# Kernel tuning notes

Hardware: AMD Instinct MI355X
Metric: run time of the kernel (lower is better)

## Reference

```python
import jax, jax.numpy as jnp
import numpy as np

SIZE = 1024        # number of neurons
INPUT = 1024       # input_size (previous layer width)
CTX = 512          # context_size
CMS = 4            # context_map_size -> 2**4 = 16 weight rows per neuron
BATCH = 256
LR = 0.01
PCLIP = 0.01       # pred_clipping
WCLIP = 5.0        # weight_clipping


def _logit(x):
    return jnp.log(x) - jnp.log1p(-x)


def setup_inputs() -> dict:
    key = jax.random.key(0)
    k1, k2, k3, k4, k5, k6 = jax.random.split(key, 6)
    logits = jax.random.normal(k1, (INPUT, BATCH), jnp.float32)
    context_inputs = jax.random.normal(k2, (CTX, BATCH), jnp.float32)
    targets = jax.random.uniform(k3, (BATCH,), jnp.float32)
    context_maps = jax.random.normal(k4, (SIZE, CMS, CTX), jnp.float32)
    context_maps = context_maps / jnp.linalg.norm(context_maps, axis=2, keepdims=True)
    context_bias = jax.random.normal(k5, (SIZE, CMS, 1), jnp.float32)
    lo = _logit(jnp.float32(PCLIP))
    hi = _logit(jnp.float32(1.0 - PCLIP))
    bias = jax.random.uniform(k6, (1,), jnp.float32, lo, hi)
    weights = jnp.full((SIZE, 2 ** CMS, INPUT), 1.0 / INPUT, jnp.float32)
    return dict(logits=logits, context_inputs=context_inputs, targets=targets,
                weights=weights, context_maps=context_maps,
                context_bias=context_bias, bias=bias)


def reference(logits, context_inputs, targets, weights, context_maps, context_bias, bias):
    # --- context hashing: which of the 2^CMS weight rows each (neuron, sample) uses ---
    # distances: (size, cms, batch)
    distances = jnp.einsum('smc,cb->smb', context_maps, context_inputs)
    bits = (distances > context_bias).astype(jnp.int32)
    conv = (2 ** jnp.arange(CMS, dtype=jnp.int32))[None, :, None]
    idx = jnp.sum(bits * conv, axis=1)                 # (size, batch) in [0, 2^CMS)

    rows = jnp.arange(SIZE)[:, None]                   # (size, 1)
    sel = weights[rows, idx]                           # gathered weights (size, batch, input)

    lo = _logit(jnp.float32(PCLIP))
    hi = _logit(jnp.float32(1.0 - PCLIP))
    # torch does matmul(sel, logits).diagonal(dim1=1,dim2=2); the diagonal is exactly
    # the per-sample dot product, computed here directly without the (size,b,b) waste.
    out = jnp.clip(jnp.einsum('sbi,ib->sb', sel, logits), lo, hi)
    out = out.at[0].set(bias[0])                       # bias overrides neuron 0

    # --- online weight update (targets provided) ---
    sig = jax.nn.sigmoid(out)                          # (size, batch)
    upd = LR * (sig - targets[None, :])[:, :, None] * logits.T[None, :, :]  # (size,b,input)
    new_weights = weights.at[rows, idx].set(jnp.clip(sel - upd, -WCLIP, WCLIP))

    return jnp.squeeze(out), new_weights
```

## Files before the change

kernel.cpp:

```cpp
#include <hip/hip_runtime.h>

#define LRC   0.01f
#define WCLIP 5.0f
#define LO   (-4.5951198501345898f)
#define HI   ( 4.5951198501345898f)

__device__ __forceinline__ unsigned short f2bf(float f) {
    unsigned int u = __float_as_uint(f);
    u += 0x7fffu + ((u >> 16) & 1u);
    return (unsigned short)(u >> 16);
}
__device__ __forceinline__ float bflo(unsigned int p) { return __uint_as_float(p << 16); }
__device__ __forceinline__ float bfhi(unsigned int p) { return __uint_as_float(p & 0xffff0000u); }

__global__ __launch_bounds__(256) void k1_idx_lt(
    const float* __restrict__ cmap,
    const float* __restrict__ ctx,
    const float* __restrict__ cbias,
    const float* __restrict__ logits,
    int*   __restrict__ idxb,
    float* __restrict__ lT)
{
    __shared__ __align__(16) float As[64 * 68];
    __shared__ __align__(16) float Bs[64 * 68];
    const int t   = threadIdx.x;
    const int blk = blockIdx.x;

    if (blk < 256) {
        const int gm = blk >> 2, gn = blk & 3;
        const int m0 = gm << 6, n0 = gn << 6;
        const int tm = t >> 4, tn = t & 15;

        const int rs = t >> 4;
        const int cs = (t & 15) << 2;

        float acc[4][4];
        #pragma unroll
        for (int i = 0; i < 4; i++)
            #pragma unroll
            for (int j = 0; j < 4; j++) acc[i][j] = 0.f;

        float4 va[4], vb[4];
        #pragma unroll
        for (int rep = 0; rep < 4; rep++) {
            va[rep] = *(const float4*)(cmap + (m0 + (rep << 4) + rs) * 512 + cs);
            vb[rep] = *(const float4*)(ctx + (((rep << 4) + rs)) * 256 + n0 + cs);
        }

        for (int k0 = 0; k0 < 512; k0 += 64) {
            __syncthreads();
            #pragma unroll
            for (int rep = 0; rep < 4; rep++) {
                const int r = (rep << 4) + rs;
                As[(cs + 0) * 68 + r] = va[rep].x;
                As[(cs + 1) * 68 + r] = va[rep].y;
                As[(cs + 2) * 68 + r] = va[rep].z;
                As[(cs + 3) * 68 + r] = va[rep].w;
                *(float4*)(Bs + r * 68 + cs) = vb[rep];
            }
            if (k0 + 64 < 512) {
                #pragma unroll
                for (int rep = 0; rep < 4; rep++) {
                    va[rep] = *(const float4*)(cmap + (m0 + (rep << 4) + rs) * 512 + k0 + 64 + cs);
                    vb[rep] = *(const float4*)(ctx + (k0 + 64 + (rep << 4) + rs) * 256 + n0 + cs);
                }
            }
            __syncthreads();

            const float* ap = As + (tm << 2);
            const float* bp = Bs + (tn << 2);
            #pragma unroll 8
            for (int k = 0; k < 64; ++k) {
                float4 a4 = *(const float4*)(ap + k * 68);
                float4 b4 = *(const float4*)(bp + k * 68);
                acc[0][0] = fmaf(a4.x, b4.x, acc[0][0]);
                acc[0][1] = fmaf(a4.x, b4.y, acc[0][1]);
                acc[0][2] = fmaf(a4.x, b4.z, acc[0][2]);
                acc[0][3] = fmaf(a4.x, b4.w, acc[0][3]);
                acc[1][0] = fmaf(a4.y, b4.x, acc[1][0]);
                acc[1][1] = fmaf(a4.y, b4.y, acc[1][1]);
                acc[1][2] = fmaf(a4.y, b4.z, acc[1][2]);
                acc[1][3] = fmaf(a4.y, b4.w, acc[1][3]);
                acc[2][0] = fmaf(a4.z, b4.x, acc[2][0]);
                acc[2][1] = fmaf(a4.z, b4.y, acc[2][1]);
                acc[2][2] = fmaf(a4.z, b4.z, acc[2][2]);
                acc[2][3] = fmaf(a4.z, b4.w, acc[2][3]);
                acc[3][0] = fmaf(a4.w, b4.x, acc[3][0]);
                acc[3][1] = fmaf(a4.w, b4.y, acc[3][1]);
                acc[3][2] = fmaf(a4.w, b4.z, acc[3][2]);
                acc[3][3] = fmaf(a4.w, b4.w, acc[3][3]);
            }
        }
        const int s = (gm << 4) + tm;
        int4 iv;
        int* ivp = &iv.x;
        float cb[4];
        #pragma unroll
        for (int i = 0; i < 4; i++) cb[i] = cbias[(s << 2) + i];
        #pragma unroll
        for (int j = 0; j < 4; j++) {
            int v = 0;
            #pragma unroll
            for (int i = 0; i < 4; i++)
                v |= (acc[i][j] > cb[i]) ? (1 << i) : 0;
            ivp[j] = v;
        }
        *(int4*)(idxb + s * 256 + n0 + (tn << 2)) = iv;
    } else {
        float* T = As;
        const int bi = blk - 256;
        const int i0 = (bi >> 2) << 6;
        const int b0 = (bi & 3) << 6;
        #pragma unroll
        for (int rep = 0; rep < 4; rep++) {
            int flat4 = rep * 256 + t;
            int r = flat4 >> 4;
            int c = (flat4 & 15) << 2;
            float4 v = *(const float4*)(logits + (i0 + r) * 256 + b0 + c);
            T[(c + 0) * 68 + r] = v.x;
            T[(c + 1) * 68 + r] = v.y;
            T[(c + 2) * 68 + r] = v.z;
            T[(c + 3) * 68 + r] = v.w;
        }
        __syncthreads();
        #pragma unroll
        for (int rep = 0; rep < 4; rep++) {
            int flat4 = rep * 256 + t;
            int r = flat4 >> 4;
            int c = (flat4 & 15) << 2;
            *(float4*)(lT + (b0 + r) * 1024 + i0 + c) =
                *(const float4*)(T + r * 68 + c);
        }
    }
}

#define WSTRIDE 514

__global__ __launch_bounds__(1024, 8) void k2_fwd_upd(
    const float* __restrict__ logits,
    const float* __restrict__ targets,
    const float* __restrict__ weights,
    const float* __restrict__ bias,
    const int*   __restrict__ idxb,
    const float* __restrict__ lT,
    float* __restrict__ outp,
    float* __restrict__ outw)
{
    __shared__ __align__(16) unsigned int wlds[32 * WSTRIDE];
    __shared__ float red[3 * 2 * 256];
    __shared__ float sig_lds[2 * 256];
    __shared__ int   lastb[32];
    __shared__ float cf_lds[32];

    const int t  = threadIdx.x;
    const int b  = t & 255;
    const int q  = t >> 8;
    const int s0 = blockIdx.x << 1;

    if (t < 32) lastb[t] = -1;

    int jg[2], rowoff[2];
    #pragma unroll
    for (int g = 0; g < 2; g++) {
        jg[g] = idxb[(s0 + g) * 256 + b];
        rowoff[g] = ((g << 4) + jg[g]) * WSTRIDE;
    }

    #pragma unroll
    for (int seg = 0; seg < 8; ++seg) {
        const int flat4 = (seg << 10) + t;
        const int r  = flat4 >> 8;
        const int c4 = (flat4 & 255) << 2;
        float4 v = *(const float4*)(weights +
                      ((size_t)(s0 + (r >> 4)) << 14) + ((r & 15) << 10) + c4);
        unsigned int p0 = (unsigned int)f2bf(v.x) | ((unsigned int)f2bf(v.y) << 16);
        unsigned int p1 = (unsigned int)f2bf(v.z) | ((unsigned int)f2bf(v.w) << 16);
        *(uint2*)(wlds + r * WSTRIDE + (c4 >> 1)) = make_uint2(p0, p1);
    }
    __syncthreads();

    float acc[2] = {0.f, 0.f};
    const int qq = q << 4;
    for (int c0 = 0; c0 < 16; ++c0) {
        const int ibase = (c0 << 6) + qq;
        #pragma unroll
        for (int ii = 0; ii < 16; ii += 4) {
            const int i = ibase + ii;
            float l0 = logits[(i + 0) * 256 + b];
            float l1 = logits[(i + 1) * 256 + b];
            float l2 = logits[(i + 2) * 256 + b];
            float l3 = logits[(i + 3) * 256 + b];
            #pragma unroll
            for (int g = 0; g < 2; g++) {
                uint2 wp = *(const uint2*)(wlds + rowoff[g] + (i >> 1));
                acc[g] = fmaf(bflo(wp.x), l0, acc[g]);
                acc[g] = fmaf(bfhi(wp.x), l1, acc[g]);
                acc[g] = fmaf(bflo(wp.y), l2, acc[g]);
                acc[g] = fmaf(bfhi(wp.y), l3, acc[g]);
            }
        }
    }

    if (q > 0) {
        #pragma unroll
        for (int g = 0; g < 2; g++) red[((q - 1) * 2 + g) * 256 + b] = acc[g];
    }
    __syncthreads();
    if (q == 0) {
        #pragma unroll
        for (int g = 0; g < 2; g++) {
            float tot = acc[g] + red[(0 * 2 + g) * 256 + b]
                               + red[(1 * 2 + g) * 256 + b]
                               + red[(2 * 2 + g) * 256 + b];
            float outv = fminf(fmaxf(tot, LO), HI);
            if (s0 + g == 0) outv = bias[0];
            outp[(s0 + g) * 256 + b] = outv;
            sig_lds[(g << 8) + b] = 1.f / (1.f + __expf(-outv));
            atomicMax(&lastb[(g << 4) + jg[g]], b);
        }
    }
    __syncthreads();
    if (t < 32) {
        int g  = t >> 4;
        int bb = lastb[t];
        float cfv = 0.f;
        if (bb >= 0) cfv = LRC * (sig_lds[(g << 8) + bb] - targets[bb]);
        cf_lds[t] = cfv;
    }
    __syncthreads();

    const int er = t >> 5;
    const int ec = (t & 31) << 2;
    const size_t rowbase = ((size_t)(s0 + (er >> 4)) << 14) + ((size_t)(er & 15) << 10);
    const int   col = lastb[er];
    const float cf  = cf_lds[er];
    const float* lrow = lT + ((size_t)(col < 0 ? 0 : col) << 10);
    const unsigned int* wrow = wlds + er * WSTRIDE;
    #pragma unroll 4
    for (int seg = 0; seg < 8; ++seg) {
        const int c2 = ec + (seg << 7);
        uint2 wp = *(const uint2*)(wrow + (c2 >> 1));
        float4 res = make_float4(bflo(wp.x), bfhi(wp.x), bflo(wp.y), bfhi(wp.y));
        if (col >= 0) {
            float4 lv = *(const float4*)(lrow + c2);
            res.x = fminf(fmaxf(res.x - cf * lv.x, -WCLIP), WCLIP);
            res.y = fminf(fmaxf(res.y - cf * lv.y, -WCLIP), WCLIP);
            res.z = fminf(fmaxf(res.z - cf * lv.z, -WCLIP), WCLIP);
            res.w = fminf(fmaxf(res.w - cf * lv.w, -WCLIP), WCLIP);
        }
        *(float4*)(outw + rowbase + c2) = res;
    }
}

extern "C" void kernel_launch(void* const* d_in, const int* in_sizes, int n_in,
                              void* d_out, int out_size, void* d_ws, size_t ws_size,
                              hipStream_t stream) {
    const float* logits  = (const float*)d_in[0];
    const float* ctx     = (const float*)d_in[1];
    const float* targets = (const float*)d_in[2];
    const float* weights = (const float*)d_in[3];
    const float* cmap    = (const float*)d_in[4];
    const float* cbias   = (const float*)d_in[5];
    const float* bias    = (const float*)d_in[6];

    float* outp = (float*)d_out;
    float* outw = outp + 1024 * 256;

    char* ws = (char*)d_ws;
    int*   idxb = (int*)ws;
    float* lT   = (float*)(ws + (1 << 20));

    k1_idx_lt <<<320, 256, 0, stream>>>(cmap, ctx, cbias, logits, idxb, lT);
    k2_fwd_upd<<<512, 1024, 0, stream>>>(logits, targets, weights, bias, idxb,
                                         lT, outp, outw);
}
```

Measured before the change: 186.9 us.

## Retile context GEMM to 64x32 and give each k2 thread two samples

The first kernel's context-hash GEMM now uses 64x32 output tiles across 512 blocks instead of 64x64 across 256, giving more blocks to spread over the CUs. In the forward kernel each thread now handles two batch samples with float2 logit loads and a software-prefetched next group, and the input dimension is split eight ways with a two-stage LDS reduction. The aim is to raise parallelism in k1 and halve redundant logit loads per weight read in k2, in exchange for extra reduction syncs and more registers.

```diff
diff --git a/kernel.cpp b/kernel.cpp
--- a/kernel.cpp
+++ b/kernel.cpp
@@ -22,30 +22,31 @@
     float* __restrict__ lT)
 {
     __shared__ __align__(16) float As[64 * 68];
-    __shared__ __align__(16) float Bs[64 * 68];
+    __shared__ __align__(16) float Bs[64 * 36];
     const int t   = threadIdx.x;
     const int blk = blockIdx.x;
 
-    if (blk < 256) {
-        const int gm = blk >> 2, gn = blk & 3;
-        const int m0 = gm << 6, n0 = gn << 6;
+    if (blk < 512) {
+        const int gm = blk >> 3, gn = blk & 7;
+        const int m0 = gm << 6, n0 = gn << 5;
         const int tm = t >> 4, tn = t & 15;
 
         const int rs = t >> 4;
         const int cs = (t & 15) << 2;
-
-        float acc[4][4];
-        #pragma unroll
-        for (int i = 0; i < 4; i++)
-            #pragma unroll
-            for (int j = 0; j < 4; j++) acc[i][j] = 0.f;
-
-        float4 va[4], vb[4];
-        #pragma unroll
-        for (int rep = 0; rep < 4; rep++) {
+        const int br = t >> 3;
+        const int bc = (t & 7) << 2;
+
+        float acc[4][2];
+        #pragma unroll
+        for (int i = 0; i < 4; i++) { acc[i][0] = 0.f; acc[i][1] = 0.f; }
+
+        float4 va[4], vb[2];
+        #pragma unroll
+        for (int rep = 0; rep < 4; rep++)
             va[rep] = *(const float4*)(cmap + (m0 + (rep << 4) + rs) * 512 + cs);
-            vb[rep] = *(const float4*)(ctx + (((rep << 4) + rs)) * 256 + n0 + cs);
-        }
+        #pragma unroll
+        for (int rep = 0; rep < 2; rep++)
+            vb[rep] = *(const float4*)(ctx + ((rep << 5) + br) * 256 + n0 + bc);
 
         for (int k0 = 0; k0 < 512; k0 += 64) {
             __syncthreads();
@@ -56,59 +57,54 @@
                 As[(cs + 1) * 68 + r] = va[rep].y;
                 As[(cs + 2) * 68 + r] = va[rep].z;
                 As[(cs + 3) * 68 + r] = va[rep].w;
-                *(float4*)(Bs + r * 68 + cs) = vb[rep];
             }
+            #pragma unroll
+            for (int rep = 0; rep < 2; rep++)
+                *(float4*)(Bs + ((rep << 5) + br) * 36 + bc) = vb[rep];
             if (k0 + 64 < 512) {
                 #pragma unroll
-                for (int rep = 0; rep < 4; rep++) {
+                for (int rep = 0; rep < 4; rep++)
                     va[rep] = *(const float4*)(cmap + (m0 + (rep << 4) + rs) * 512 + k0 + 64 + cs);
-                    vb[rep] = *(const float4*)(ctx + (k0 + 64 + (rep << 4) + rs) * 256 + n0 + cs);
-                }
+                #pragma unroll
+                for (int rep = 0; rep < 2; rep++)
+                    vb[rep] = *(const float4*)(ctx + (k0 + 64 + (rep << 5) + br) * 256 + n0 + bc);
             }
             __syncthreads();
 
             const float* ap = As + (tm << 2);
-            const float* bp = Bs + (tn << 2);
+            const float* bp = Bs + (tn << 1);
             #pragma unroll 8
             for (int k = 0; k < 64; ++k) {
                 float4 a4 = *(const float4*)(ap + k * 68);
-                float4 b4 = *(const float4*)(bp + k * 68);
-                acc[0][0] = fmaf(a4.x, b4.x, acc[0][0]);
-                acc[0][1] = fmaf(a4.x, b4.y, acc[0][1]);
-                acc[0][2] = fmaf(a4.x, b4.z, acc[0][2]);
-                acc[0][3] = fmaf(a4.x, b4.w, acc[0][3]);
-                acc[1][0] = fmaf(a4.y, b4.x, acc[1][0]);
-                acc[1][1] = fmaf(a4.y, b4.y, acc[1][1]);
-                acc[1][2] = fmaf(a4.y, b4.z, acc[1][2]);
-                acc[1][3] = fmaf(a4.y, b4.w, acc[1][3]);
-                acc[2][0] = fmaf(a4.z, b4.x, acc[2][0]);
-                acc[2][1] = fmaf(a4.z, b4.y, acc[2][1]);
-                acc[2][2] = fmaf(a4.z, b4.z, acc[2][2]);
-                acc[2][3] = fmaf(a4.z, b4.w, acc[2][3]);
-                acc[3][0] = fmaf(a4.w, b4.x, acc[3][0]);
-                acc[3][1] = fmaf(a4.w, b4.y, acc[3][1]);
-                acc[3][2] = fmaf(a4.w, b4.z, acc[3][2]);
-                acc[3][3] = fmaf(a4.w, b4.w, acc[3][3]);
+                float2 b2 = *(const float2*)(bp + k * 36);
+                acc[0][0] = fmaf(a4.x, b2.x, acc[0][0]);
+                acc[0][1] = fmaf(a4.x, b2.y, acc[0][1]);
+                acc[1][0] = fmaf(a4.y, b2.x, acc[1][0]);
+                acc[1][1] = fmaf(a4.y, b2.y, acc[1][1]);
+                acc[2][0] = fmaf(a4.z, b2.x, acc[2][0]);
+                acc[2][1] = fmaf(a4.z, b2.y, acc[2][1]);
+                acc[3][0] = fmaf(a4.w, b2.x, acc[3][0]);
+                acc[3][1] = fmaf(a4.w, b2.y, acc[3][1]);
             }
         }
         const int s = (gm << 4) + tm;
-        int4 iv;
+        float cb[4];
+        #pragma unroll
+        for (int i = 0; i < 4; i++) cb[i] = cbias[(s << 2) + i];
+        int2 iv;
         int* ivp = &iv.x;
-        float cb[4];
-        #pragma unroll
-        for (int i = 0; i < 4; i++) cb[i] = cbias[(s << 2) + i];
-        #pragma unroll
-        for (int j = 0; j < 4; j++) {
+        #pragma unroll
+        for (int j = 0; j < 2; j++) {
             int v = 0;
             #pragma unroll
             for (int i = 0; i < 4; i++)
                 v |= (acc[i][j] > cb[i]) ? (1 << i) : 0;
             ivp[j] = v;
         }
-        *(int4*)(idxb + s * 256 + n0 + (tn << 2)) = iv;
+        *(int2*)(idxb + s * 256 + n0 + (tn << 1)) = iv;
     } else {
         float* T = As;
-        const int bi = blk - 256;
+        const int bi = blk - 512;
         const int i0 = (bi >> 2) << 6;
         const int b0 = (bi & 3) << 6;
         #pragma unroll
@@ -147,23 +143,26 @@
     float* __restrict__ outw)
 {
     __shared__ __align__(16) unsigned int wlds[32 * WSTRIDE];
-    __shared__ float red[3 * 2 * 256];
+    __shared__ float red[4 * 2 * 256];
     __shared__ float sig_lds[2 * 256];
     __shared__ int   lastb[32];
     __shared__ float cf_lds[32];
 
     const int t  = threadIdx.x;
-    const int b  = t & 255;
-    const int q  = t >> 8;
+    const int bp = t & 127;
+    const int b0 = bp << 1;
+    const int o  = t >> 7;
     const int s0 = blockIdx.x << 1;
 
     if (t < 32) lastb[t] = -1;
 
-    int jg[2], rowoff[2];
+    int jg[2][2], ro[2][2];
     #pragma unroll
     for (int g = 0; g < 2; g++) {
-        jg[g] = idxb[(s0 + g) * 256 + b];
-        rowoff[g] = ((g << 4) + jg[g]) * WSTRIDE;
+        int2 jv = *(const int2*)(idxb + (s0 + g) * 256 + b0);
+        jg[g][0] = jv.x;  jg[g][1] = jv.y;
+        ro[g][0] = ((g << 4) + jv.x) * WSTRIDE;
+        ro[g][1] = ((g << 4) + jv.y) * WSTRIDE;
     }
 
     #pragma unroll
@@ -179,44 +178,87 @@
     }
     __syncthreads();
 
-    float acc[2] = {0.f, 0.f};
-    const int qq = q << 4;
-    for (int c0 = 0; c0 < 16; ++c0) {
-        const int ibase = (c0 << 6) + qq;
-        #pragma unroll
-        for (int ii = 0; ii < 16; ii += 4) {
-            const int i = ibase + ii;
-            float l0 = logits[(i + 0) * 256 + b];
-            float l1 = logits[(i + 1) * 256 + b];
-            float l2 = logits[(i + 2) * 256 + b];
-            float l3 = logits[(i + 3) * 256 + b];
-            #pragma unroll
-            for (int g = 0; g < 2; g++) {
-                uint2 wp = *(const uint2*)(wlds + rowoff[g] + (i >> 1));
-                acc[g] = fmaf(bflo(wp.x), l0, acc[g]);
-                acc[g] = fmaf(bfhi(wp.x), l1, acc[g]);
-                acc[g] = fmaf(bflo(wp.y), l2, acc[g]);
-                acc[g] = fmaf(bfhi(wp.y), l3, acc[g]);
-            }
-        }
-    }
-
-    if (q > 0) {
-        #pragma unroll
-        for (int g = 0; g < 2; g++) red[((q - 1) * 2 + g) * 256 + b] = acc[g];
-    }
-    __syncthreads();
-    if (q == 0) {
+    const float2* lbase = (const float2*)logits + bp;
+    const int i0 = o << 7;
+
+    float acc00 = 0.f, acc01 = 0.f, acc10 = 0.f, acc11 = 0.f;
+    float2 c0 = lbase[(i0 + 0) * 128];
+    float2 c1 = lbase[(i0 + 1) * 128];
+    float2 c2 = lbase[(i0 + 2) * 128];
+    float2 c3 = lbase[(i0 + 3) * 128];
+
+    #pragma unroll 4
+    for (int ii = 0; ii < 128; ii += 4) {
+        const int ipn = (ii < 124) ? (i0 + ii + 4) : (i0 + 124);
+        float2 n0 = lbase[(ipn + 0) * 128];
+        float2 n1 = lbase[(ipn + 1) * 128];
+        float2 n2 = lbase[(ipn + 2) * 128];
+        float2 n3 = lbase[(ipn + 3) * 128];
+
+        const int ch = (i0 + ii) >> 1;
+        uint2 w00 = *(const uint2*)(wlds + ro[0][0] + ch);
+        uint2 w01 = *(const uint2*)(wlds + ro[0][1] + ch);
+        uint2 w10 = *(const uint2*)(wlds + ro[1][0] + ch);
+        uint2 w11 = *(const uint2*)(wlds + ro[1][1] + ch);
+
+        acc00 = fmaf(bflo(w00.x), c0.x, acc00);
+        acc00 = fmaf(bfhi(w00.x), c1.x, acc00);
+        acc00 = fmaf(bflo(w00.y), c2.x, acc00);
+        acc00 = fmaf(bfhi(w00.y), c3.x, acc00);
+
+        acc01 = fmaf(bflo(w01.x), c0.y, acc01);
+        acc01 = fmaf(bfhi(w01.x), c1.y, acc01);
+        acc01 = fmaf(bflo(w01.y), c2.y, acc01);
+        acc01 = fmaf(bfhi(w01.y), c3.y, acc01);
+
+        acc10 = fmaf(bflo(w10.x), c0.x, acc10);
+        acc10 = fmaf(bfhi(w10.x), c1.x, acc10);
+        acc10 = fmaf(bflo(w10.y), c2.x, acc10);
+        acc10 = fmaf(bfhi(w10.y), c3.x, acc10);
+
+        acc11 = fmaf(bflo(w11.x), c0.y, acc11);
+        acc11 = fmaf(bfhi(w11.x), c1.y, acc11);
+        acc11 = fmaf(bflo(w11.y), c2.y, acc11);
+        acc11 = fmaf(bfhi(w11.y), c3.y, acc11);
+
+        c0 = n0; c1 = n1; c2 = n2; c3 = n3;
+    }
+
+    if (o >= 4) {
+        *(float2*)(red + (((o - 4) << 1) + 0) * 256 + b0) = make_float2(acc00, acc01);
+        *(float2*)(red + (((o - 4) << 1) + 1) * 256 + b0) = make_float2(acc10, acc11);
+    }
+    __syncthreads();
+    if (o < 4) {
+        float2 r0 = *(const float2*)(red + ((o << 1) + 0) * 256 + b0);
+        float2 r1 = *(const float2*)(red + ((o << 1) + 1) * 256 + b0);
+        acc00 += r0.x; acc01 += r0.y;
+        acc10 += r1.x; acc11 += r1.y;
+    }
+    __syncthreads();
+    if (o >= 1 && o < 4) {
+        *(float2*)(red + (((o - 1) << 1) + 0) * 256 + b0) = make_float2(acc00, acc01);
+        *(float2*)(red + (((o - 1) << 1) + 1) * 256 + b0) = make_float2(acc10, acc11);
+    }
+    __syncthreads();
+    if (o == 0) {
         #pragma unroll
         for (int g = 0; g < 2; g++) {
-            float tot = acc[g] + red[(0 * 2 + g) * 256 + b]
-                               + red[(1 * 2 + g) * 256 + b]
-                               + red[(2 * 2 + g) * 256 + b];
-            float outv = fminf(fmaxf(tot, LO), HI);
-            if (s0 + g == 0) outv = bias[0];
-            outp[(s0 + g) * 256 + b] = outv;
-            sig_lds[(g << 8) + b] = 1.f / (1.f + __expf(-outv));
-            atomicMax(&lastb[(g << 4) + jg[g]], b);
+            float ax = (g == 0) ? acc00 : acc10;
+            float ay = (g == 0) ? acc01 : acc11;
+            float2 r0 = *(const float2*)(red + ((0 << 1) + g) * 256 + b0);
+            float2 r1 = *(const float2*)(red + ((1 << 1) + g) * 256 + b0);
+            float2 r2 = *(const float2*)(red + ((2 << 1) + g) * 256 + b0);
+            float tx = ax + r0.x + r1.x + r2.x;
+            float ty = ay + r0.y + r1.y + r2.y;
+            float ox = fminf(fmaxf(tx, LO), HI);
+            float oy = fminf(fmaxf(ty, LO), HI);
+            if (s0 + g == 0) { ox = bias[0]; oy = bias[0]; }
+            *(float2*)(outp + (s0 + g) * 256 + b0) = make_float2(ox, oy);
+            sig_lds[(g << 8) + b0 + 0] = 1.f / (1.f + __expf(-ox));
+            sig_lds[(g << 8) + b0 + 1] = 1.f / (1.f + __expf(-oy));
+            atomicMax(&lastb[(g << 4) + jg[g][0]], b0 + 0);
+            atomicMax(&lastb[(g << 4) + jg[g][1]], b0 + 1);
         }
     }
     __syncthreads();
@@ -270,7 +312,7 @@
     int*   idxb = (int*)ws;
     float* lT   = (float*)(ws + (1 << 20));
 
-    k1_idx_lt <<<320, 256, 0, stream>>>(cmap, ctx, cbias, logits, idxb, lT);
+    k1_idx_lt <<<576, 256, 0, stream>>>(cmap, ctx, cbias, logits, idxb, lT);
     k2_fwd_upd<<<512, 1024, 0, stream>>>(logits, targets, weights, bias, idxb,
                                          lT, outp, outw);
 }
```

After: 196.5 us. +5.1%, slower.

## Compute forward dot products per wavefront over samples using transposed logits and shuffles

Applied to the files above, without the earlier changes.

The forward pass changes from one thread per sample with four thread groups splitting the input dimension (plus an LDS reduction) to one wavefront per sample. Each lane reads contiguous float4 slices of the transposed logits and 128-bit chunks of the selected bf16 weight row, and the partial sums are combined with a cross-lane shuffle reduction. This replaces strided scalar global logits loads and the LDS reduction buffer with coalesced vector loads. The LDS row padding is removed so rows are 16-byte aligned, which may add bank conflicts when different samples in a wavefront select different rows.

```diff
diff --git a/kernel.cpp b/kernel.cpp
--- a/kernel.cpp
+++ b/kernel.cpp
@@ -5,10 +5,10 @@
 #define LO   (-4.5951198501345898f)
 #define HI   ( 4.5951198501345898f)
 
-__device__ __forceinline__ unsigned short f2bf(float f) {
+__device__ __forceinline__ unsigned int f2bf(float f) {
     unsigned int u = __float_as_uint(f);
     u += 0x7fffu + ((u >> 16) & 1u);
-    return (unsigned short)(u >> 16);
+    return (u >> 16);
 }
 __device__ __forceinline__ float bflo(unsigned int p) { return __uint_as_float(p << 16); }
 __device__ __forceinline__ float bfhi(unsigned int p) { return __uint_as_float(p & 0xffff0000u); }
@@ -134,7 +134,7 @@
     }
 }
 
-#define WSTRIDE 514
+#define WSTRIDE 512
 
 __global__ __launch_bounds__(1024, 8) void k2_fwd_upd(
     const float* __restrict__ logits,
@@ -147,24 +147,14 @@
     float* __restrict__ outw)
 {
     __shared__ __align__(16) unsigned int wlds[32 * WSTRIDE];
-    __shared__ float red[3 * 2 * 256];
     __shared__ float sig_lds[2 * 256];
     __shared__ int   lastb[32];
     __shared__ float cf_lds[32];
 
     const int t  = threadIdx.x;
-    const int b  = t & 255;
-    const int q  = t >> 8;
     const int s0 = blockIdx.x << 1;
 
     if (t < 32) lastb[t] = -1;
-
-    int jg[2], rowoff[2];
-    #pragma unroll
-    for (int g = 0; g < 2; g++) {
-        jg[g] = idxb[(s0 + g) * 256 + b];
-        rowoff[g] = ((g << 4) + jg[g]) * WSTRIDE;
-    }
 
     #pragma unroll
     for (int seg = 0; seg < 8; ++seg) {
@@ -173,53 +163,72 @@
         const int c4 = (flat4 & 255) << 2;
         float4 v = *(const float4*)(weights +
                       ((size_t)(s0 + (r >> 4)) << 14) + ((r & 15) << 10) + c4);
-        unsigned int p0 = (unsigned int)f2bf(v.x) | ((unsigned int)f2bf(v.y) << 16);
-        unsigned int p1 = (unsigned int)f2bf(v.z) | ((unsigned int)f2bf(v.w) << 16);
+        unsigned int p0 = f2bf(v.x) | (f2bf(v.y) << 16);
+        unsigned int p1 = f2bf(v.z) | (f2bf(v.w) << 16);
         *(uint2*)(wlds + r * WSTRIDE + (c4 >> 1)) = make_uint2(p0, p1);
     }
     __syncthreads();
 
-    float acc[2] = {0.f, 0.f};
-    const int qq = q << 4;
-    for (int c0 = 0; c0 < 16; ++c0) {
-        const int ibase = (c0 << 6) + qq;
-        #pragma unroll
-        for (int ii = 0; ii < 16; ii += 4) {
-            const int i = ibase + ii;
-            float l0 = logits[(i + 0) * 256 + b];
-            float l1 = logits[(i + 1) * 256 + b];
-            float l2 = logits[(i + 2) * 256 + b];
-            float l3 = logits[(i + 3) * 256 + b];
-            #pragma unroll
-            for (int g = 0; g < 2; g++) {
-                uint2 wp = *(const uint2*)(wlds + rowoff[g] + (i >> 1));
-                acc[g] = fmaf(bflo(wp.x), l0, acc[g]);
-                acc[g] = fmaf(bfhi(wp.x), l1, acc[g]);
-                acc[g] = fmaf(bflo(wp.y), l2, acc[g]);
-                acc[g] = fmaf(bfhi(wp.y), l3, acc[g]);
-            }
-        }
-    }
-
-    if (q > 0) {
-        #pragma unroll
-        for (int g = 0; g < 2; g++) red[((q - 1) * 2 + g) * 256 + b] = acc[g];
+    const int wv   = t >> 6;
+    const int lane = t & 63;
+    const float bias0 = bias[0];
+
+    for (int bb = 0; bb < 16; ++bb) {
+        const int b = (wv << 4) + bb;
+
+        const float4* lrow = (const float4*)(lT + ((size_t)b << 10)) + (lane << 1);
+        float4 l0 = lrow[0];
+        float4 l1 = lrow[1];
+        float4 l2 = lrow[128];
+        float4 l3 = lrow[129];
+
+        const int j0 = idxb[(size_t)s0 * 256 + b];
+        const int j1 = idxb[(size_t)(s0 + 1) * 256 + b];
+        const uint4* wr0 = (const uint4*)(wlds + j0 * WSTRIDE) + lane;
+        const uint4* wr1 = (const uint4*)(wlds + (16 + j1) * WSTRIDE) + lane;
+        uint4 wa0 = wr0[0], wb0 = wr0[64];
+        uint4 wa1 = wr1[0], wb1 = wr1[64];
+
+        float p0 = 0.f, q0 = 0.f, p1 = 0.f, q1 = 0.f;
+        p0 = fmaf(bflo(wa0.x), l0.x, p0); p0 = fmaf(bfhi(wa0.x), l0.y, p0);
+        p0 = fmaf(bflo(wa0.y), l0.z, p0); p0 = fmaf(bfhi(wa0.y), l0.w, p0);
+        p0 = fmaf(bflo(wa0.z), l1.x, p0); p0 = fmaf(bfhi(wa0.z), l1.y, p0);
+        p0 = fmaf(bflo(wa0.w), l1.z, p0); p0 = fmaf(bfhi(wa0.w), l1.w, p0);
+        q0 = fmaf(bflo(wb0.x), l2.x, q0); q0 = fmaf(bfhi(wb0.x), l2.y, q0);
+        q0 = fmaf(bflo(wb0.y), l2.z, q0); q0 = fmaf(bfhi(wb0.y), l2.w, q0);
+        q0 = fmaf(bflo(wb0.z), l3.x, q0); q0 = fmaf(bfhi(wb0.z), l3.y, q0);
+        q0 = fmaf(bflo(wb0.w), l3.z, q0); q0 = fmaf(bfhi(wb0.w), l3.w, q0);
+        p1 = fmaf(bflo(wa1.x), l0.x, p1); p1 = fmaf(bfhi(wa1.x), l0.y, p1);
+        p1 = fmaf(bflo(wa1.y), l0.z, p1); p1 = fmaf(bfhi(wa1.y), l0.w, p1);
+        p1 = fmaf(bflo(wa1.z), l1.x, p1); p1 = fmaf(bfhi(wa1.z), l1.y, p1);
+        p1 = fmaf(bflo(wa1.w), l1.z, p1); p1 = fmaf(bfhi(wa1.w), l1.w, p1);
+        q1 = fmaf(bflo(wb1.x), l2.x, q1); q1 = fmaf(bfhi(wb1.x), l2.y, q1);
+        q1 = fmaf(bflo(wb1.y), l2.z, q1); q1 = fmaf(bfhi(wb1.y), l2.w, q1);
+        q1 = fmaf(bflo(wb1.z), l3.x, q1); q1 = fmaf(bfhi(wb1.z), l3.y, q1);
+        q1 = fmaf(bflo(wb1.w), l3.z, q1); q1 = fmaf(bfhi(wb1.w), l3.w, q1);
+
+        float v0 = p0 + q0;
+        float v1 = p1 + q1;
+        #pragma unroll
+        for (int m = 32; m > 0; m >>= 1) {
+            v0 += __shfl_xor(v0, m, 64);
+            v1 += __shfl_xor(v1, m, 64);
+        }
+
+        if (lane == 0) {
+            float o0 = fminf(fmaxf(v0, LO), HI);
+            float o1 = fminf(fmaxf(v1, LO), HI);
+            if (s0 == 0) o0 = bias0;
+            outp[(size_t)s0 * 256 + b]       = o0;
+            outp[(size_t)(s0 + 1) * 256 + b] = o1;
+            sig_lds[b]       = 1.f / (1.f + __expf(-o0));
+            sig_lds[256 + b] = 1.f / (1.f + __expf(-o1));
+            atomicMax(&lastb[j0], b);
+            atomicMax(&lastb[16 + j1], b);
+        }
     }
     __syncthreads();
-    if (q == 0) {
-        #pragma unroll
-        for (int g = 0; g < 2; g++) {
-            float tot = acc[g] + red[(0 * 2 + g) * 256 + b]
-                               + red[(1 * 2 + g) * 256 + b]
-                               + red[(2 * 2 + g) * 256 + b];
-            float outv = fminf(fmaxf(tot, LO), HI);
-            if (s0 + g == 0) outv = bias[0];
-            outp[(s0 + g) * 256 + b] = outv;
-            sig_lds[(g << 8) + b] = 1.f / (1.f + __expf(-outv));
-            atomicMax(&lastb[(g << 4) + jg[g]], b);
-        }
-    }
-    __syncthreads();
+
     if (t < 32) {
         int g  = t >> 4;
         int bb = lastb[t];
```

New measurement: 198.5 us. 1.06x slower.
